# Kernel optimization log

Measured on AMD Instinct MI355X. Metric: run time of the kernel, lower is better.

Reference implementation:

```python
import jax, jax.numpy as jnp
from jax import lax
import numpy as np

# (cin, cout, kernel, pad) for the 18 convs (funs 1,3,5,6,7,9,10,11,13..17,19..23)
CONVS = [(3,32,3,0),(32,64,3,0),(64,128,3,1),(128,64,1,0),(64,128,3,1),
         (128,256,3,1),(256,128,1,0),(128,256,3,0),(256,512,3,1),(512,256,1,0),
         (256,512,3,1),(512,256,1,0),(256,512,3,0),(512,256,3,1),(256,128,1,0),
         (128,64,3,1),(64,32,1,0),(32,6,3,1)]
# maxpool(2,2) after conv index (1-based) -> pool padding (torch pads with -inf, floor mode)
POOL_AFTER = {1: 1, 2: 1, 5: 0, 8: 1, 13: 1}
GT = (0.567, 0.469, 0.206, 0.53)  # hardcoded ground-truth box (cx, cy, w, h), normalized


def _backbone(x, ws, bs):
    for i, (w, b) in enumerate(zip(ws, bs), 1):
        pad = CONVS[i - 1][3]
        x = lax.conv_general_dilated(
            x, w, (1, 1), [(pad, pad), (pad, pad)],
            dimension_numbers=("NCHW", "OIHW", "NCHW")) + b[None, :, None, None]
        if i in POOL_AFTER:
            p = POOL_AFTER[i]
            x = lax.reduce_window(
                x, -jnp.inf, lax.max, (1, 1, 2, 2), (1, 1, 2, 2),
                [(0, 0), (0, 0), (p, p), (p, p)])
    return x


def _head(x):
    # torch: x.transpose(1,3) on [B,6,H,W] -> [B,W,H,6]; j indexes W, k indexes H
    xt = jnp.transpose(x, (0, 3, 2, 1))
    B, W, H, _ = xt.shape
    j = jnp.arange(W, dtype=xt.dtype)[None, :, None]  # [1,W,1]
    k = jnp.arange(H, dtype=xt.dtype)[None, None, :]  # [1,1,H]
    px = (j + xt[..., 2]) / W
    py = (k + xt[..., 3]) / H
    pw = jnp.exp(xt[..., 4]) / W
    ph = jnp.exp(xt[..., 5]) / H
    # center-format IoU against the single gt box (detached mask, as in torch via float())
    iw = jnp.clip(jnp.minimum(px + pw * 0.5, GT[0] + GT[2] * 0.5)
                  - jnp.maximum(px - pw * 0.5, GT[0] - GT[2] * 0.5), 0.0)
    ih = jnp.clip(jnp.minimum(py + ph * 0.5, GT[1] + GT[3] * 0.5)
                  - jnp.maximum(py - ph * 0.5, GT[1] - GT[3] * 0.5), 0.0)
    inter = iw * ih
    iou = inter / (pw * ph + GT[2] * GT[3] - inter)
    iou = lax.stop_gradient(iou)
    tx = GT[0] * W - j          # [1,W,1]
    ty = GT[1] * H - k          # [1,1,H]
    tw = np.log(GT[2] * W).astype(np.float32)
    th = np.log(GT[3] * H).astype(np.float32)
    l1 = (jnp.abs(tx - xt[..., 2]) + jnp.abs(ty - xt[..., 3])
          + jnp.abs(tw - xt[..., 4]) + jnp.abs(th - xt[..., 5]))
    loss = jnp.sum(jnp.where(iou > 0.5, l1, 0.0)).reshape(1)
    return xt, loss


def setup_inputs() -> dict:
    key = jax.random.key(0)
    keys = jax.random.split(key, 1 + 2 * len(CONVS))
    d = {"x": jax.random.normal(keys[0], (16, 3, 416, 416), jnp.float32)}
    for i, (cin, cout, ks, _) in enumerate(CONVS, 1):
        fan_in = cin * ks * ks
        d[f"w{i}"] = jax.random.normal(keys[2 * i - 1], (cout, cin, ks, ks), jnp.float32) / np.sqrt(fan_in)
        d[f"b{i}"] = jax.random.normal(keys[2 * i], (cout,), jnp.float32) * 0.01
    return d


def reference(x, w1, b1, w2, b2, w3, b3, w4, b4, w5, b5, w6, b6, w7, b7, w8, b8,
              w9, b9, w10, b10, w11, b11, w12, b12, w13, b13, w14, b14, w15, b15,
              w16, b16, w17, b17, w18, b18):
    ws = [w1, w2, w3, w4, w5, w6, w7, w8, w9, w10, w11, w12, w13, w14, w15, w16, w17, w18]
    bs = [b1, b2, b3, b4, b5, b6, b7, b8, b9, b10, b11, b12, b13, b14, b15, b16, b17, b18]
    feat = _backbone(x, ws, bs)
    xt, loss = _head(feat)
    return (xt, loss)
```

## Files before the change

kernel.cpp:

```cpp
#include <hip/hip_runtime.h>
#include <math.h>

typedef short v8s __attribute__((ext_vector_type(8)));
typedef float v4f __attribute__((ext_vector_type(4)));

template<int K, int COT, bool POOL, bool MASK, bool SWAP>
__global__ __launch_bounds__(256) void conv_fused(
    const float* __restrict__ in, const float* __restrict__ wgt,
    const float* __restrict__ bias, float* __restrict__ out,
    int B, int Cin, int Hin, int Win,
    int Hc, int Wc, int Hout, int Wout,
    int Cout, int cpad, int ppad,
    int inPS, int inRS, int inOfs, int outPS, int outRS, int outOfs)
{
    constexpr int NPY = POOL ? 2 : 1;
    constexpr int PS  = K + NPY - 1;
    const int spatial = Hout * Wout;
    const int idx = (SWAP ? blockIdx.y : blockIdx.x) * blockDim.x + threadIdx.x;
    const int cog = SWAP ? blockIdx.x : blockIdx.y;
    const int total = B * spatial;
    if (idx >= total) return;
    const int b  = idx / spatial;
    const int sp = idx - b * spatial;
    const int oy = sp / Wout;
    const int ox = sp - oy * Wout;
    const int co0 = cog * COT;

    const int cy0 = POOL ? (2 * oy - ppad) : oy;
    const int cx0 = POOL ? (2 * ox - ppad) : ox;
    const int iy0 = cy0 - cpad;
    const int ix0 = cx0 - cpad;

    bool my[PS], mx[PS];
#pragma unroll
    for (int i = 0; i < PS; i++) {
        my[i] = !MASK || ((unsigned)(iy0 + i) < (unsigned)Hin);
        mx[i] = !MASK || ((unsigned)(ix0 + i) < (unsigned)Win);
    }

    float acc[COT][NPY * NPY];
#pragma unroll
    for (int c = 0; c < COT; c++)
#pragma unroll
        for (int p = 0; p < NPY * NPY; p++) acc[c][p] = 0.f;

    const float* inB = in + inOfs + (size_t)b * Cin * inPS;
    const long wBase  = (long)co0 * Cin * K * K;

    for (int ci = 0; ci < Cin; ci++) {
        const float* ip = inB + (size_t)ci * inPS;
        float patch[PS][PS];
#pragma unroll
        for (int py = 0; py < PS; py++) {
#pragma unroll
            for (int px = 0; px < PS; px++) {
                float v = 0.f;
                if (my[py] && mx[px]) v = ip[(iy0 + py) * inRS + (ix0 + px)];
                patch[py][px] = v;
            }
        }
        const float* wp = wgt + wBase + (long)ci * K * K;
#pragma unroll
        for (int c = 0; c < COT; c++) {
#pragma unroll
            for (int kh = 0; kh < K; kh++)
#pragma unroll
            for (int kw = 0; kw < K; kw++) {
                const float wv = wp[(long)c * Cin * K * K + kh * K + kw];
#pragma unroll
                for (int dy = 0; dy < NPY; dy++)
#pragma unroll
                for (int dx = 0; dx < NPY; dx++)
                    acc[c][dy * NPY + dx] = fmaf(wv, patch[dy + kh][dx + kw],
                                                 acc[c][dy * NPY + dx]);
            }
        }
    }

#pragma unroll
    for (int c = 0; c < COT; c++) {
        float v;
        if (POOL) {
            v = -INFINITY;
#pragma unroll
            for (int dy = 0; dy < NPY; dy++)
#pragma unroll
            for (int dx = 0; dx < NPY; dx++) {
                const int cy = cy0 + dy, cx = cx0 + dx;
                if ((unsigned)cy < (unsigned)Hc && (unsigned)cx < (unsigned)Wc)
                    v = fmaxf(v, acc[c][dy * NPY + dx]);
            }
        } else {
            v = acc[c][0];
        }
        v += bias[co0 + c];
        out[outOfs + (size_t)(b * Cout + co0 + c) * outPS + oy * outRS + ox] = v;
    }
}

__global__ __launch_bounds__(256) void ring_zero(
    float* __restrict__ buf, int planes, int H, int W)
{
    int Wp = W + 2, Hp = H + 2;
    int ringlen = 2 * Wp + 2 * H;
    int t = blockIdx.x * 256 + threadIdx.x;
    if (t >= planes * ringlen) return;
    int p = t / ringlen, r = t - p * ringlen;
    float* pl = buf + (size_t)p * Hp * Wp;
    int idx;
    if (r < Wp) idx = r;
    else if (r < 2 * Wp) idx = (Hp - 1) * Wp + (r - Wp);
    else { int rr = r - 2 * Wp; int row = 1 + (rr >> 1); idx = row * Wp + ((rr & 1) ? (Wp - 1) : 0); }
    pl[idx] = 0.f;
}

__device__ __forceinline__ unsigned short f2bf_rne(float x) {
    unsigned u = __float_as_uint(x);
    return (unsigned short)((u + 0x7fffu + ((u >> 16) & 1u)) >> 16);
}
__device__ __forceinline__ float bf2f(unsigned short h) {
    return __uint_as_float(((unsigned)h) << 16);
}

__global__ __launch_bounds__(256) void prepack(
    const float* __restrict__ w, unsigned short* __restrict__ hi,
    unsigned short* __restrict__ lo, int cout, int kdim, int nkb)
{
    int t = blockIdx.x * 256 + threadIdx.x;
    if (t >= cout * kdim) return;
    int co = t / kdim, k = t - co * kdim;
    int cb = co >> 4, m = co & 15, kb = k >> 5, kk = k & 31;
    int lane = ((kk >> 3) << 4) | m, j = kk & 7;
    long dst = ((long)(cb * nkb + kb) << 9) + lane * 8 + j;
    float x = w[t];
    unsigned short h = f2bf_rne(x);
    hi[dst] = h;
    lo[dst] = f2bf_rne(x - bf2f(h));
}

template<int MT, int KS, bool SPLIT>
__global__ __launch_bounds__(256) void conv_mfma(
    const float* __restrict__ in, const unsigned short* __restrict__ whi,
    const unsigned short* __restrict__ wlo, const float* __restrict__ bias,
    float* __restrict__ out, int Cin, int inHWp, int inWp, int Hc, int Wc,
    int Cout, int pad, int b0, int nb, int nkbTot, int nkbPer, int Mpad,
    int outHWp, int outWp)
{
    const int HW = Hc * Wc;
    const int M = nb * HW;
    const int tid = threadIdx.x;
    const int lane = tid & 63;
    const int wv = tid >> 6;
    const int spBase = blockIdx.x * 64;
    const int kb0 = SPLIT ? blockIdx.z * nkbPer : 0;
    const int kb1 = SPLIT ? kb0 + nkbPer : nkbTot;

    __shared__ unsigned short P[2][5120];

    const int spoL = lane >> 2;
    int kkc[2];
    kkc[0] = (tid & 3) + 4 * wv;
    kkc[1] = kkc[0] + 16;

    const float* sptr[4];
    int soff[4];
#pragma unroll
    for (int j = 0; j < 4; ++j) {
        int sp = spBase + spoL + 16 * j;
        int q = sp < M ? sp : M - 1;
        int b = q / HW; int r = q - b * HW;
        int soy = r / Wc, sox = r - soy * Wc;
        soff[j] = (soy + 1) * inWp + (sox + 1);
        sptr[j] = in + (size_t)(b0 + b) * Cin * inHWp;
    }

    int ci[2], r9[2], koff[2];
#pragma unroll
    for (int m = 0; m < 2; ++m) {
        int k = kb0 * 32 + kkc[m];
        if (KS == 3) {
            ci[m] = k / 9; r9[m] = k - 9 * ci[m];
            int d3 = (r9[m] >= 3) + (r9[m] >= 6);
            koff[m] = ci[m] * inHWp + (d3 - pad) * inWp + (r9[m] - 3 * d3 - pad);
        } else { ci[m] = k; koff[m] = k * inHWp; }
    }

    float rv[8];
#define STAGE()                                                                \
    {                                                                          \
        _Pragma("unroll")                                                      \
        for (int m = 0; m < 2; ++m)                                            \
        _Pragma("unroll")                                                      \
        for (int j = 0; j < 4; ++j)                                            \
            rv[m * 4 + j] = sptr[j][koff[m] + soff[j]];                        \
    }
#define ADVANCE()                                                              \
    {                                                                          \
        _Pragma("unroll")                                                      \
        for (int m = 0; m < 2; ++m) {                                          \
            if (KS == 3) {                                                     \
                r9[m] += 5; int c = r9[m] >= 9; r9[m] -= c ? 9 : 0;            \
                ci[m] += 3 + c;                                                \
                int d3 = (r9[m] >= 3) + (r9[m] >= 6);                          \
                koff[m] = ci[m] * inHWp + (d3 - pad) * inWp                    \
                        + (r9[m] - 3 * d3 - pad);                              \
            } else { koff[m] += 32 * inHWp; }                                  \
        }                                                                      \
    }

    STAGE();

    const int g0 = blockIdx.y * (MT * 4) + wv * MT;
    const unsigned short* whp[MT];
    const unsigned short* wlp[MT];
#pragma unroll
    for (int mt = 0; mt < MT; ++mt) {
        size_t base = (((size_t)(g0 + mt) * nkbTot + kb0) << 9) + lane * 8;
        whp[mt] = whi + base; wlp[mt] = wlo + base;
    }

    v4f acc[MT][4];
    {
        v4f z = {0.f, 0.f, 0.f, 0.f};
#pragma unroll
        for (int mt = 0; mt < MT; ++mt)
#pragma unroll
            for (int nt = 0; nt < 4; ++nt) acc[mt][nt] = z;
    }

    for (int kb = kb0; kb < kb1; ++kb) {
        unsigned short* Ph = P[kb & 1];
#pragma unroll
        for (int m = 0; m < 2; ++m)
#pragma unroll
        for (int j = 0; j < 4; ++j) {
            float v = rv[m * 4 + j];
            unsigned vb = __float_as_uint(v);
            float res = v - __uint_as_float(vb & 0xffff0000u);
            int a = (spoL + 16 * j) * 40 + kkc[m];
            Ph[a] = (unsigned short)(vb >> 16);
            Ph[2560 + a] = (unsigned short)(__float_as_uint(res) >> 16);
        }
        __syncthreads();

        v8s wh[MT], wl[MT];
#pragma unroll
        for (int mt = 0; mt < MT; ++mt) {
            wh[mt] = *(const v8s*)whp[mt];
            wl[mt] = *(const v8s*)wlp[mt];
            whp[mt] += 512; wlp[mt] += 512;
        }

        if (kb + 1 < kb1) { ADVANCE(); STAGE(); }

#pragma unroll
        for (int nt = 0; nt < 4; ++nt) {
            int ro = (nt * 16 + (lane & 15)) * 40 + (lane >> 4) * 8;
            v8s ph = *(const v8s*)(Ph + ro);
            v8s pl = *(const v8s*)(Ph + 2560 + ro);
#pragma unroll
            for (int mt = 0; mt < MT; ++mt) {
                acc[mt][nt] = __builtin_amdgcn_mfma_f32_16x16x32_bf16(wh[mt], ph, acc[mt][nt], 0, 0, 0);
                acc[mt][nt] = __builtin_amdgcn_mfma_f32_16x16x32_bf16(wh[mt], pl, acc[mt][nt], 0, 0, 0);
                acc[mt][nt] = __builtin_amdgcn_mfma_f32_16x16x32_bf16(wl[mt], ph, acc[mt][nt], 0, 0, 0);
            }
        }
    }
#undef STAGE
#undef ADVANCE

    const int qrow = (lane >> 4) * 4;
    if (SPLIT) {
        float* pz = out + (size_t)blockIdx.z * Cout * Mpad;
#pragma unroll
        for (int mt = 0; mt < MT; ++mt) {
            int co = (g0 + mt) * 16 + qrow;
#pragma unroll
            for (int nt = 0; nt < 4; ++nt) {
                int sp = spBase + nt * 16 + (lane & 15);
                if (sp < M) {
#pragma unroll
                    for (int r = 0; r < 4; ++r)
                        pz[(size_t)(co + r) * Mpad + sp] = acc[mt][nt][r];
                }
            }
        }
    } else {
#pragma unroll
        for (int mt = 0; mt < MT; ++mt) {
            int co = (g0 + mt) * 16 + qrow;
            float bsv[4];
#pragma unroll
            for (int r = 0; r < 4; ++r) bsv[r] = bias[co + r];
#pragma unroll
            for (int nt = 0; nt < 4; ++nt) {
                int sp = spBase + nt * 16 + (lane & 15);
                if (sp < M) {
                    int b = sp / HW, rsp = sp - b * HW;
                    int y = rsp / Wc, xx = rsp - y * Wc;
                    float* op = out + (size_t)(b * Cout + co) * outHWp
                              + (size_t)(y + 1) * outWp + (xx + 1);
#pragma unroll
                    for (int r = 0; r < 4; ++r)
                        op[(size_t)r * outHWp] = acc[mt][nt][r] + bsv[r];
                }
            }
        }
    }
}

__global__ __launch_bounds__(256) void sk_reduce(
    const float* __restrict__ part, const float* __restrict__ bias,
    float* __restrict__ out, int Cout, int HW, int Wc, int M, int Mpad, int SK,
    int outHWp, int outWp)
{
    int t = blockIdx.x * 256 + threadIdx.x;
    if (t >= Cout * M) return;
    int co = t / M, m = t - co * M;
    float s = bias[co];
    for (int k = 0; k < SK; ++k)
        s += part[((size_t)k * Cout + co) * Mpad + m];
    int b = m / HW, rsp = m - b * HW;
    int y = rsp / Wc, xx = rsp - y * Wc;
    out[(size_t)(b * Cout + co) * outHWp + (size_t)(y + 1) * outWp + (xx + 1)] = s;
}

__global__ __launch_bounds__(256) void maxpool_k(
    const float* __restrict__ in, float* __restrict__ out,
    int Hc, int Wc, int Hp, int Wp, int p, int total,
    int inHWp, int inWp, int outHWp, int outWp)
{
    int t = blockIdx.x * 256 + threadIdx.x;
    if (t >= total) return;
    int wp2 = Hp * Wp;
    int bc = t / wp2; int r = t - bc * wp2;
    int y = r / Wp, xx = r - y * Wp;
    int y0 = 2 * y - p, x0 = 2 * xx - p;
    const float* ip = in + (size_t)bc * inHWp;
    float v = -INFINITY;
#pragma unroll
    for (int dy = 0; dy < 2; ++dy)
#pragma unroll
    for (int dx = 0; dx < 2; ++dx) {
        int yy = y0 + dy, xc = x0 + dx;
        if ((unsigned)yy < (unsigned)Hc && (unsigned)xc < (unsigned)Wc)
            v = fmaxf(v, ip[(yy + 1) * inWp + (xc + 1)]);
    }
    out[(size_t)bc * outHWp + (size_t)(y + 1) * outWp + (xx + 1)] = v;
}

__global__ __launch_bounds__(1024) void head_kernel(
    const float* __restrict__ x, float* __restrict__ out, int B)
{
    const int W = 13, H = 13;
    const float gx = 0.567f, gy = 0.469f, gw = 0.206f, gh = 0.53f;
    const int tid = threadIdx.x;
    const int total = B * W * H;
    float lsum = 0.f;
    for (int i = tid; i < total; i += blockDim.x) {
        const int b = i / (W * H);
        const int r = i - b * W * H;
        const int j = r / H;
        const int k = r - j * H;
        float v[6];
#pragma unroll
        for (int c = 0; c < 6; c++) {
            v[c] = x[((b * 6 + c) * H + k) * W + j];
            out[((b * W + j) * H + k) * 6 + c] = v[c];
        }
        const float px = (j + v[2]) / (float)W;
        const float py = (k + v[3]) / (float)H;
        const float pw = expf(v[4]) / (float)W;
        const float ph = expf(v[5]) / (float)H;
        float iw = fminf(px + pw * 0.5f, gx + gw * 0.5f)
                 - fmaxf(px - pw * 0.5f, gx - gw * 0.5f);
        iw = fmaxf(iw, 0.f);
        float ih = fminf(py + ph * 0.5f, gy + gh * 0.5f)
                 - fmaxf(py - ph * 0.5f, gy - gh * 0.5f);
        ih = fmaxf(ih, 0.f);
        const float inter = iw * ih;
        const float iou = inter / (pw * ph + gw * gh - inter);
        const float tx = gx * W - (float)j;
        const float ty = gy * H - (float)k;
        const float tw = logf(gw * W);
        const float th = logf(gh * H);
        const float l1 = fabsf(tx - v[2]) + fabsf(ty - v[3])
                       + fabsf(tw - v[4]) + fabsf(th - v[5]);
        if (iou > 0.5f) lsum += l1;
    }
    __shared__ float red[1024];
    red[tid] = lsum;
    __syncthreads();
    for (int s = blockDim.x / 2; s > 0; s >>= 1) {
        if (tid < s) red[tid] += red[tid + s];
        __syncthreads();
    }
    if (tid == 0) out[total * 6] = red[0];
}

extern "C" void kernel_launch(void* const* d_in, const int* in_sizes, int n_in,
                              void* d_out, int out_size, void* d_ws, size_t ws_size,
                              hipStream_t stream)
{
    (void)in_sizes; (void)n_in; (void)out_size;
    const float* x = (const float*)d_in[0];
    const int B = 16;
    const size_t MB = 1024 * 1024;
    char* ws = (char*)d_ws;
    float* bufA = (float*)ws;
    float* bufB = (float*)(ws + 93 * MB);
    unsigned short* WHI = (unsigned short*)(ws + 141 * MB);
    unsigned short* WLO = (unsigned short*)(ws + 153 * MB);
    char* TEMP = ws + 165 * MB;
    const bool gemmOK = ws_size >= 166 * MB;
    const size_t tempAvail = ws_size > 165 * MB ? ws_size - 165 * MB : 0;

    static const struct { int cin, cout, ks, cpad, pool, ppad; } L[18] = {
        {3,  32, 3, 0, 1, 1}, {32, 64, 3, 0, 1, 1}, {64, 128, 3, 1, 0, 0},
        {128, 64, 1, 0, 0, 0}, {64, 128, 3, 1, 1, 0}, {128, 256, 3, 1, 0, 0},
        {256, 128, 1, 0, 0, 0}, {128, 256, 3, 0, 1, 1}, {256, 512, 3, 1, 0, 0},
        {512, 256, 1, 0, 0, 0}, {256, 512, 3, 1, 0, 0}, {512, 256, 1, 0, 0, 0},
        {256, 512, 3, 0, 1, 1}, {512, 256, 3, 1, 0, 0}, {256, 128, 1, 0, 0, 0},
        {128, 64, 3, 1, 0, 0}, {64, 32, 1, 0, 0, 0}, {32, 6, 3, 1, 0, 0}
    };
    static const bool RING[18] = {0,1,0,1,1,0,0,1,0,1,0,0,1,0,1,0,1,0};

    if (gemmOK) {
        size_t off = 0;
        for (int i = 1; i <= 15; ++i) {
            int kdim = L[i].cin * L[i].ks * L[i].ks;
            int n = L[i].cout * kdim;
            prepack<<<(n + 255) / 256, 256, 0, stream>>>(
                (const float*)d_in[2 * i + 1], WHI + off, WLO + off,
                L[i].cout, kdim, kdim / 32);
            off += (size_t)n;
        }
    }

    const float* cur = x;
    int Hin = 416, Win = 416;
    size_t woff = 0;

    for (int i = 0; i < 18; ++i) {
        const auto& l = L[i];
        const int Hc = Hin + 2 * l.cpad - l.ks + 1;
        const int Wc = Win + 2 * l.cpad - l.ks + 1;
        const int Hout = l.pool ? (Hc + 2 * l.ppad - 2) / 2 + 1 : Hc;
        const int Wout = l.pool ? (Wc + 2 * l.ppad - 2) / 2 + 1 : Wc;
        float* dst = (i % 2 == 0) ? bufA : bufB;
        const float* w  = (const float*)d_in[2 * i + 1];
        const float* bb = (const float*)d_in[2 * i + 2];
        const int kdim = l.cin * l.ks * l.ks;
        const int nkb = kdim / 32;

        const int inRS  = (i == 0) ? Win : (Win + 2);
        const int inPS  = (i == 0) ? Hin * Win : (Hin + 2) * (Win + 2);
        const int inOfs = (i == 0) ? 0 : (inRS + 1);
        const bool outPad = (i != 17);
        const int outRS  = outPad ? (Wout + 2) : Wout;
        const int outPS  = outPad ? (Hout + 2) * (Wout + 2) : Hout * Wout;
        const int outOfs = outPad ? (outRS + 1) : 0;
        const int tRS = Wc + 2, tPS = (Hc + 2) * (Wc + 2);

        if (RING[i]) {
            int planes = B * l.cout;
            int ringlen = 2 * (Wout + 2) + 2 * Hout;
            ring_zero<<<(planes * ringlen + 255) / 256, 256, 0, stream>>>(
                dst, planes, Hout, Wout);
        }

        int nb = 16;
        if (l.pool) {
            size_t perImg = (size_t)l.cout * tPS * 4;
            while (nb && perImg * (size_t)nb > tempAvail) nb >>= 1;
        }
        const bool useG = gemmOK && i >= 1 && i <= 15 && (!l.pool || nb >= 1);

        if (useG) {
            for (int b0 = 0; b0 < B; b0 += nb) {
                const int M = nb * Hc * Wc;
                const int gx = (M + 63) / 64;
                int MTv = (l.cout >= 256 && (long)gx * (l.cout / 256) >= 512) ? 4
                        : (l.cout >= 128 && (long)gx * (l.cout / 128) >= 512) ? 2 : 1;
                int gy = l.cout / (MTv * 64);
                int SK = 1;
                if (!l.pool && (long)gx * gy < 512) {
                    if (nkb % 4 == 0 && (size_t)4 * l.cout * gx * 64 * 4 <= tempAvail) SK = 4;
                    else if (nkb % 2 == 0 && (size_t)2 * l.cout * gx * 64 * 4 <= tempAvail) SK = 2;
                }
                const int nkbPer = nkb / SK;
                const int Mpad = gx * 64;
                float* gout = l.pool ? (float*)TEMP : (SK > 1 ? (float*)TEMP : dst);
                const int gHWp = l.pool ? tPS : (SK > 1 ? 0 : outPS);
                const int gWp  = l.pool ? tRS : (SK > 1 ? 0 : outRS);
                dim3 gr(gx, gy, SK);
#define GL(MTC, KSC, SPL)                                                      \
                conv_mfma<MTC, KSC, SPL><<<gr, 256, 0, stream>>>(              \
                    cur, WHI + woff, WLO + woff, bb, gout, l.cin, inPS, inRS,  \
                    Hc, Wc, l.cout, l.cpad, b0, nb, nkb, nkbPer, Mpad,         \
                    gHWp, gWp)
#define G2(MTC, KSC) do { if (SK > 1) GL(MTC, KSC, true); else GL(MTC, KSC, false); } while (0)
                if (MTv == 4)      { if (l.ks == 3) G2(4, 3); else G2(4, 1); }
                else if (MTv == 2) { if (l.ks == 3) G2(2, 3); else G2(2, 1); }
                else               { if (l.ks == 3) G2(1, 3); else G2(1, 1); }
#undef G2
#undef GL
                if (SK > 1) {
                    int tot = l.cout * M;
                    sk_reduce<<<(tot + 255) / 256, 256, 0, stream>>>(
                        (const float*)TEMP, bb, dst, l.cout, Hc * Wc, Wc, M,
                        Mpad, SK, outPS, outRS);
                }
                if (l.pool) {
                    int total = nb * l.cout * Hout * Wout;
                    maxpool_k<<<(total + 255) / 256, 256, 0, stream>>>(
                        (const float*)TEMP,
                        dst + (size_t)b0 * l.cout * outPS,
                        Hc, Wc, Hout, Wout, l.ppad, total, tPS, tRS, outPS, outRS);
                }
            }
        } else {
            const int spatial = Hout * Wout;
#define FL(KK, CC, PP, MM, SW)                                                 \
            conv_fused<KK, CC, PP, MM, SW><<<                                  \
                SW ? dim3(l.cout / CC, (B * spatial + 255) / 256)              \
                   : dim3((B * spatial + 255) / 256, l.cout / CC),             \
                256, 0, stream>>>(                                             \
                cur, w, bb, dst, B, l.cin, Hin, Win, Hc, Wc, Hout, Wout,       \
                l.cout, l.cpad, l.ppad, inPS, inRS, inOfs, outPS, outRS, outOfs)
            if (i == 0)                           FL(3, 8, true, true, true);
            else if (i == 16)                     FL(1, 8, false, false, false);
            else if (i == 17)                     FL(3, 6, false, false, false);
            else if (l.pool)                      FL(3, 4, true, true, false);
            else if (l.ks == 3)                   FL(3, 8, false, true, false);
            else                                  FL(1, 8, false, true, false);
#undef FL
        }

        if (i >= 1 && i <= 15) woff += (size_t)l.cout * kdim;
        cur = dst;
        Hin = Hout;
        Win = Wout;
    }

    head_kernel<<<1, 1024, 0, stream>>>(cur, (float*)d_out, B);
}
```

Measured before the change: 1.520 ms.

## Prefetch high weights a chunk ahead, pack LDS stores, rework tile and split-K selection

New measurement: 1.650 ms. +8.6%, slower.

```diff
diff --git a/kernel.cpp b/kernel.cpp
--- a/kernel.cpp
+++ b/kernel.cpp
@@ -157,27 +157,23 @@
 
     __shared__ unsigned short P[2][5120];
 
-    const int spoL = lane >> 2;
-    int kkc[2];
-    kkc[0] = (tid & 3) + 4 * wv;
-    kkc[1] = kkc[0] + 16;
-
-    const float* sptr[4];
-    int soff[4];
+    const int spo = lane >> 2;
+    const int kp  = (tid & 3) + 4 * wv;
+
+    int jbase[4];
 #pragma unroll
     for (int j = 0; j < 4; ++j) {
-        int sp = spBase + spoL + 16 * j;
+        int sp = spBase + spo + 16 * j;
         int q = sp < M ? sp : M - 1;
         int b = q / HW; int r = q - b * HW;
         int soy = r / Wc, sox = r - soy * Wc;
-        soff[j] = (soy + 1) * inWp + (sox + 1);
-        sptr[j] = in + (size_t)(b0 + b) * Cin * inHWp;
+        jbase[j] = (b0 + b) * Cin * inHWp + (soy + 1) * inWp + (sox + 1);
     }
 
     int ci[2], r9[2], koff[2];
 #pragma unroll
     for (int m = 0; m < 2; ++m) {
-        int k = kb0 * 32 + kkc[m];
+        int k = kb0 * 32 + 2 * kp + m;
         if (KS == 3) {
             ci[m] = k / 9; r9[m] = k - 9 * ci[m];
             int d3 = (r9[m] >= 3) + (r9[m] >= 6);
@@ -192,7 +188,7 @@
         for (int m = 0; m < 2; ++m)                                            \
         _Pragma("unroll")                                                      \
         for (int j = 0; j < 4; ++j)                                            \
-            rv[m * 4 + j] = sptr[j][koff[m] + soff[j]];                        \
+            rv[m * 4 + j] = in[jbase[j] + koff[m]];                            \
     }
 #define ADVANCE()                                                              \
     {                                                                          \
@@ -219,6 +215,10 @@
         whp[mt] = whi + base; wlp[mt] = wlo + base;
     }
 
+    v8s WHa[MT], WHb[MT];
+#pragma unroll
+    for (int mt = 0; mt < MT; ++mt) { WHa[mt] = *(const v8s*)whp[mt]; whp[mt] += 512; }
+
     v4f acc[MT][4];
     {
         v4f z = {0.f, 0.f, 0.f, 0.f};
@@ -228,44 +228,65 @@
             for (int nt = 0; nt < 4; ++nt) acc[mt][nt] = z;
     }
 
-    for (int kb = kb0; kb < kb1; ++kb) {
-        unsigned short* Ph = P[kb & 1];
-#pragma unroll
-        for (int m = 0; m < 2; ++m)
-#pragma unroll
-        for (int j = 0; j < 4; ++j) {
-            float v = rv[m * 4 + j];
-            unsigned vb = __float_as_uint(v);
-            float res = v - __uint_as_float(vb & 0xffff0000u);
-            int a = (spoL + 16 * j) * 40 + kkc[m];
-            Ph[a] = (unsigned short)(vb >> 16);
-            Ph[2560 + a] = (unsigned short)(__float_as_uint(res) >> 16);
-        }
-        __syncthreads();
-
-        v8s wh[MT], wl[MT];
-#pragma unroll
-        for (int mt = 0; mt < MT; ++mt) {
-            wh[mt] = *(const v8s*)whp[mt];
-            wl[mt] = *(const v8s*)wlp[mt];
-            whp[mt] += 512; wlp[mt] += 512;
-        }
-
-        if (kb + 1 < kb1) { ADVANCE(); STAGE(); }
-
-#pragma unroll
-        for (int nt = 0; nt < 4; ++nt) {
-            int ro = (nt * 16 + (lane & 15)) * 40 + (lane >> 4) * 8;
-            v8s ph = *(const v8s*)(Ph + ro);
-            v8s pl = *(const v8s*)(Ph + 2560 + ro);
-#pragma unroll
-            for (int mt = 0; mt < MT; ++mt) {
-                acc[mt][nt] = __builtin_amdgcn_mfma_f32_16x16x32_bf16(wh[mt], ph, acc[mt][nt], 0, 0, 0);
-                acc[mt][nt] = __builtin_amdgcn_mfma_f32_16x16x32_bf16(wh[mt], pl, acc[mt][nt], 0, 0, 0);
-                acc[mt][nt] = __builtin_amdgcn_mfma_f32_16x16x32_bf16(wl[mt], ph, acc[mt][nt], 0, 0, 0);
-            }
-        }
-    }
+#define CHUNK(WC, WN)                                                          \
+    {                                                                          \
+        unsigned short* Pl = P[kb & 1];                                        \
+        _Pragma("unroll")                                                      \
+        for (int j = 0; j < 4; ++j) {                                          \
+            unsigned vb0 = __float_as_uint(rv[j]);                             \
+            unsigned vb1 = __float_as_uint(rv[4 + j]);                         \
+            unsigned hiP = (vb0 >> 16) | (vb1 & 0xffff0000u);                  \
+            float r0 = rv[j]     - __uint_as_float(vb0 & 0xffff0000u);         \
+            float r1 = rv[4 + j] - __uint_as_float(vb1 & 0xffff0000u);         \
+            unsigned loP = (__float_as_uint(r0) >> 16)                         \
+                         | (__float_as_uint(r1) & 0xffff0000u);                \
+            int a = (spo + 16 * j) * 40 + 2 * kp;                              \
+            *(unsigned*)(Pl + a) = hiP;                                        \
+            *(unsigned*)(Pl + 2560 + a) = loP;                                 \
+        }                                                                      \
+        __syncthreads();                                                       \
+        v8s wl_[MT];                                                           \
+        _Pragma("unroll")                                                      \
+        for (int mt = 0; mt < MT; ++mt) {                                      \
+            wl_[mt] = *(const v8s*)wlp[mt]; wlp[mt] += 512;                    \
+        }                                                                      \
+        if (kb + 1 < kb1) {                                                    \
+            _Pragma("unroll")                                                  \
+            for (int mt = 0; mt < MT; ++mt) {                                  \
+                WN[mt] = *(const v8s*)whp[mt]; whp[mt] += 512;                 \
+            }                                                                  \
+            ADVANCE(); STAGE();                                                \
+        }                                                                      \
+        v8s phr[4];                                                            \
+        _Pragma("unroll")                                                      \
+        for (int nt = 0; nt < 4; ++nt) {                                       \
+            int ro = (nt * 16 + (lane & 15)) * 40 + (lane >> 4) * 8;           \
+            phr[nt] = *(const v8s*)(Pl + ro);                                  \
+            v8s plr = *(const v8s*)(Pl + 2560 + ro);                           \
+            _Pragma("unroll")                                                  \
+            for (int mt = 0; mt < MT; ++mt) {                                  \
+                acc[mt][nt] = __builtin_amdgcn_mfma_f32_16x16x32_bf16(         \
+                    WC[mt], phr[nt], acc[mt][nt], 0, 0, 0);                    \
+                acc[mt][nt] = __builtin_amdgcn_mfma_f32_16x16x32_bf16(         \
+                    WC[mt], plr, acc[mt][nt], 0, 0, 0);                        \
+            }                                                                  \
+        }                                                                      \
+        _Pragma("unroll")                                                      \
+        for (int nt = 0; nt < 4; ++nt)                                         \
+        _Pragma("unroll")                                                      \
+        for (int mt = 0; mt < MT; ++mt)                                        \
+            acc[mt][nt] = __builtin_amdgcn_mfma_f32_16x16x32_bf16(             \
+                wl_[mt], phr[nt], acc[mt][nt], 0, 0, 0);                       \
+    }
+
+    int kb = kb0;
+    for (;;) {
+        CHUNK(WHa, WHb);
+        if (++kb >= kb1) break;
+        CHUNK(WHb, WHa);
+        if (++kb >= kb1) break;
+    }
+#undef CHUNK
 #undef STAGE
 #undef ADVANCE
 
@@ -480,16 +501,21 @@
             for (int b0 = 0; b0 < B; b0 += nb) {
                 const int M = nb * Hc * Wc;
                 const int gx = (M + 63) / 64;
-                int MTv = (l.cout >= 256 && (long)gx * (l.cout / 256) >= 512) ? 4
-                        : (l.cout >= 128 && (long)gx * (l.cout / 128) >= 512) ? 2 : 1;
+                const int Mpad = gx * 64;
+                int MTv = (l.cout >= 256) ? 4 : (l.cout >= 128 ? 2 : 1);
                 int gy = l.cout / (MTv * 64);
                 int SK = 1;
-                if (!l.pool && (long)gx * gy < 512) {
-                    if (nkb % 4 == 0 && (size_t)4 * l.cout * gx * 64 * 4 <= tempAvail) SK = 4;
-                    else if (nkb % 2 == 0 && (size_t)2 * l.cout * gx * 64 * 4 <= tempAvail) SK = 2;
+                if (!l.pool) {
+                    while ((long)gx * gy * SK < 512 && SK < 16 &&
+                           nkb % (SK * 2) == 0 &&
+                           (size_t)(SK * 2) * l.cout * Mpad * 4 <= tempAvail)
+                        SK *= 2;
+                } else {
+                    while (MTv > 1 && (long)gx * gy < 512) {
+                        MTv >>= 1; gy = l.cout / (MTv * 64);
+                    }
                 }
                 const int nkbPer = nkb / SK;
-                const int Mpad = gx * 64;
                 float* gout = l.pool ? (float*)TEMP : (SK > 1 ? (float*)TEMP : dst);
                 const int gHWp = l.pool ? tPS : (SK > 1 ? 0 : outPS);
                 const int gWp  = l.pool ? tRS : (SK > 1 ? 0 : outRS);
```

## Add intra-block K-split across two wave groups with LDS reduction in MFMA conv

Applied to the files above, without the earlier changes.

New measurement: 1.583 ms. 4.1% more time.

```diff
diff --git a/kernel.cpp b/kernel.cpp
--- a/kernel.cpp
+++ b/kernel.cpp
@@ -138,8 +138,8 @@
     lo[dst] = f2bf_rne(x - bf2f(h));
 }
 
-template<int MT, int KS, bool SPLIT>
-__global__ __launch_bounds__(256) void conv_mfma(
+template<int MT, int KS, bool SPLIT, int KW>
+__global__ __launch_bounds__(256 * KW) void conv_mfma(
     const float* __restrict__ in, const unsigned short* __restrict__ whi,
     const unsigned short* __restrict__ wlo, const float* __restrict__ bias,
     float* __restrict__ out, int Cin, int inHWp, int inWp, int Hc, int Wc,
@@ -150,34 +150,34 @@
     const int M = nb * HW;
     const int tid = threadIdx.x;
     const int lane = tid & 63;
-    const int wv = tid >> 6;
+    const int tl  = tid & 255;
+    const int grp = tid >> 8;
+    const int wv  = (tid >> 6) & 3;
     const int spBase = blockIdx.x * 64;
     const int kb0 = SPLIT ? blockIdx.z * nkbPer : 0;
     const int kb1 = SPLIT ? kb0 + nkbPer : nkbTot;
-
-    __shared__ unsigned short P[2][5120];
-
-    const int spoL = lane >> 2;
-    int kkc[2];
-    kkc[0] = (tid & 3) + 4 * wv;
-    kkc[1] = kkc[0] + 16;
-
-    const float* sptr[4];
-    int soff[4];
+    const int half = (kb1 - kb0) / KW;
+    const int kb0g = kb0 + grp * half;
+
+    __shared__ unsigned short P[KW][2][5120];
+
+    const int spo = lane >> 2;
+    const int kp  = (tl & 3) + 4 * wv;
+
+    int jbase[4];
 #pragma unroll
     for (int j = 0; j < 4; ++j) {
-        int sp = spBase + spoL + 16 * j;
+        int sp = spBase + spo + 16 * j;
         int q = sp < M ? sp : M - 1;
         int b = q / HW; int r = q - b * HW;
         int soy = r / Wc, sox = r - soy * Wc;
-        soff[j] = (soy + 1) * inWp + (sox + 1);
-        sptr[j] = in + (size_t)(b0 + b) * Cin * inHWp;
+        jbase[j] = (b0 + b) * Cin * inHWp + (soy + 1) * inWp + (sox + 1);
     }
 
     int ci[2], r9[2], koff[2];
 #pragma unroll
     for (int m = 0; m < 2; ++m) {
-        int k = kb0 * 32 + kkc[m];
+        int k = kb0g * 32 + 2 * kp + m;
         if (KS == 3) {
             ci[m] = k / 9; r9[m] = k - 9 * ci[m];
             int d3 = (r9[m] >= 3) + (r9[m] >= 6);
@@ -192,7 +192,7 @@
         for (int m = 0; m < 2; ++m)                                            \
         _Pragma("unroll")                                                      \
         for (int j = 0; j < 4; ++j)                                            \
-            rv[m * 4 + j] = sptr[j][koff[m] + soff[j]];                        \
+            rv[m * 4 + j] = in[jbase[j] + koff[m]];                            \
     }
 #define ADVANCE()                                                              \
     {                                                                          \
@@ -215,7 +215,7 @@
     const unsigned short* wlp[MT];
 #pragma unroll
     for (int mt = 0; mt < MT; ++mt) {
-        size_t base = (((size_t)(g0 + mt) * nkbTot + kb0) << 9) + lane * 8;
+        size_t base = (((size_t)(g0 + mt) * nkbTot + kb0g) << 9) + lane * 8;
         whp[mt] = whi + base; wlp[mt] = wlo + base;
     }
 
@@ -228,36 +228,37 @@
             for (int nt = 0; nt < 4; ++nt) acc[mt][nt] = z;
     }
 
-    for (int kb = kb0; kb < kb1; ++kb) {
-        unsigned short* Ph = P[kb & 1];
-#pragma unroll
-        for (int m = 0; m < 2; ++m)
+    for (int cc = 0; cc < half; ++cc) {
+        unsigned short* Pl = (unsigned short*)P[grp][cc & 1];
 #pragma unroll
         for (int j = 0; j < 4; ++j) {
-            float v = rv[m * 4 + j];
-            unsigned vb = __float_as_uint(v);
-            float res = v - __uint_as_float(vb & 0xffff0000u);
-            int a = (spoL + 16 * j) * 40 + kkc[m];
-            Ph[a] = (unsigned short)(vb >> 16);
-            Ph[2560 + a] = (unsigned short)(__float_as_uint(res) >> 16);
+            unsigned vb0 = __float_as_uint(rv[j]);
+            unsigned vb1 = __float_as_uint(rv[4 + j]);
+            unsigned hiP = (vb0 >> 16) | (vb1 & 0xffff0000u);
+            float r0 = rv[j]     - __uint_as_float(vb0 & 0xffff0000u);
+            float r1 = rv[4 + j] - __uint_as_float(vb1 & 0xffff0000u);
+            unsigned loP = (__float_as_uint(r0) >> 16)
+                         | (__float_as_uint(r1) & 0xffff0000u);
+            int a = (spo + 16 * j) * 40 + 2 * kp;
+            *(unsigned*)(Pl + a) = hiP;
+            *(unsigned*)(Pl + 2560 + a) = loP;
         }
         __syncthreads();
 
         v8s wh[MT], wl[MT];
 #pragma unroll
         for (int mt = 0; mt < MT; ++mt) {
-            wh[mt] = *(const v8s*)whp[mt];
-            wl[mt] = *(const v8s*)wlp[mt];
-            whp[mt] += 512; wlp[mt] += 512;
-        }
-
-        if (kb + 1 < kb1) { ADVANCE(); STAGE(); }
+            wh[mt] = *(const v8s*)whp[mt]; whp[mt] += 512;
+            wl[mt] = *(const v8s*)wlp[mt]; wlp[mt] += 512;
+        }
+
+        if (cc + 1 < half) { ADVANCE(); STAGE(); }
 
 #pragma unroll
         for (int nt = 0; nt < 4; ++nt) {
             int ro = (nt * 16 + (lane & 15)) * 40 + (lane >> 4) * 8;
-            v8s ph = *(const v8s*)(Ph + ro);
-            v8s pl = *(const v8s*)(Ph + 2560 + ro);
+            v8s ph = *(const v8s*)(Pl + ro);
+            v8s pl = *(const v8s*)(Pl + 2560 + ro);
 #pragma unroll
             for (int mt = 0; mt < MT; ++mt) {
                 acc[mt][nt] = __builtin_amdgcn_mfma_f32_16x16x32_bf16(wh[mt], ph, acc[mt][nt], 0, 0, 0);
@@ -269,40 +270,66 @@
 #undef STAGE
 #undef ADVANCE
 
-    const int qrow = (lane >> 4) * 4;
-    if (SPLIT) {
-        float* pz = out + (size_t)blockIdx.z * Cout * Mpad;
-#pragma unroll
-        for (int mt = 0; mt < MT; ++mt) {
-            int co = (g0 + mt) * 16 + qrow;
-#pragma unroll
-            for (int nt = 0; nt < 4; ++nt) {
-                int sp = spBase + nt * 16 + (lane & 15);
-                if (sp < M) {
-#pragma unroll
-                    for (int r = 0; r < 4; ++r)
-                        pz[(size_t)(co + r) * Mpad + sp] = acc[mt][nt][r];
+    if (KW == 2) {
+        __syncthreads();
+        float* R = (float*)&P[0][0][0];
+        if (grp == 1) {
+#pragma unroll
+            for (int mt = 0; mt < MT; ++mt)
+#pragma unroll
+            for (int nt = 0; nt < 4; ++nt)
+#pragma unroll
+            for (int r = 0; r < 4; ++r)
+                R[((mt * 4 + nt) * 4 + r) * 256 + tl] = acc[mt][nt][r];
+        }
+        __syncthreads();
+        if (grp == 0) {
+#pragma unroll
+            for (int mt = 0; mt < MT; ++mt)
+#pragma unroll
+            for (int nt = 0; nt < 4; ++nt)
+#pragma unroll
+            for (int r = 0; r < 4; ++r)
+                acc[mt][nt][r] += R[((mt * 4 + nt) * 4 + r) * 256 + tl];
+        }
+    }
+
+    if (KW == 1 || grp == 0) {
+        const int qrow = (lane >> 4) * 4;
+        if (SPLIT) {
+            float* pz = out + (size_t)blockIdx.z * Cout * Mpad;
+#pragma unroll
+            for (int mt = 0; mt < MT; ++mt) {
+                int co = (g0 + mt) * 16 + qrow;
+#pragma unroll
+                for (int nt = 0; nt < 4; ++nt) {
+                    int sp = spBase + nt * 16 + (lane & 15);
+                    if (sp < M) {
+#pragma unroll
+                        for (int r = 0; r < 4; ++r)
+                            pz[(size_t)(co + r) * Mpad + sp] = acc[mt][nt][r];
+                    }
                 }
             }
-        }
-    } else {
-#pragma unroll
-        for (int mt = 0; mt < MT; ++mt) {
-            int co = (g0 + mt) * 16 + qrow;
-            float bsv[4];
-#pragma unroll
-            for (int r = 0; r < 4; ++r) bsv[r] = bias[co + r];
-#pragma unroll
-            for (int nt = 0; nt < 4; ++nt) {
-                int sp = spBase + nt * 16 + (lane & 15);
-                if (sp < M) {
-                    int b = sp / HW, rsp = sp - b * HW;
-                    int y = rsp / Wc, xx = rsp - y * Wc;
-                    float* op = out + (size_t)(b * Cout + co) * outHWp
-                              + (size_t)(y + 1) * outWp + (xx + 1);
-#pragma unroll
-                    for (int r = 0; r < 4; ++r)
-                        op[(size_t)r * outHWp] = acc[mt][nt][r] + bsv[r];
+        } else {
+#pragma unroll
+            for (int mt = 0; mt < MT; ++mt) {
+                int co = (g0 + mt) * 16 + qrow;
+                float bsv[4];
+#pragma unroll
+                for (int r = 0; r < 4; ++r) bsv[r] = bias[co + r];
+#pragma unroll
+                for (int nt = 0; nt < 4; ++nt) {
+                    int sp = spBase + nt * 16 + (lane & 15);
+                    if (sp < M) {
+                        int b = sp / HW, rsp = sp - b * HW;
+                        int y = rsp / Wc, xx = rsp - y * Wc;
+                        float* op = out + (size_t)(b * Cout + co) * outHWp
+                                  + (size_t)(y + 1) * outWp + (xx + 1);
+#pragma unroll
+                        for (int r = 0; r < 4; ++r)
+                            op[(size_t)r * outHWp] = acc[mt][nt][r] + bsv[r];
+                    }
                 }
             }
         }
@@ -480,30 +507,41 @@
             for (int b0 = 0; b0 < B; b0 += nb) {
                 const int M = nb * Hc * Wc;
                 const int gx = (M + 63) / 64;
-                int MTv = (l.cout >= 256 && (long)gx * (l.cout / 256) >= 512) ? 4
-                        : (l.cout >= 128 && (long)gx * (l.cout / 128) >= 512) ? 2 : 1;
+                const int Mpad = gx * 64;
+                int MTv = (l.cout >= 256) ? 4 : (l.cout >= 128 ? 2 : 1);
                 int gy = l.cout / (MTv * 64);
+                if (MTv == 4 && (long)gx * gy < 1024) { MTv = 2; gy = l.cout / 128; }
+                int KW = 1;
+                if ((long)gx * gy < 1024 && MTv <= 2 && nkb % 2 == 0) KW = 2;
                 int SK = 1;
-                if (!l.pool && (long)gx * gy < 512) {
-                    if (nkb % 4 == 0 && (size_t)4 * l.cout * gx * 64 * 4 <= tempAvail) SK = 4;
-                    else if (nkb % 2 == 0 && (size_t)2 * l.cout * gx * 64 * 4 <= tempAvail) SK = 2;
+                if (!l.pool && KW == 2 && MTv == 2) {
+                    while ((long)gx * gy * SK * KW < 512 && SK < 16 &&
+                           nkb % (SK * 2 * KW) == 0 &&
+                           (size_t)(SK * 2) * l.cout * (size_t)Mpad * 4 <= tempAvail)
+                        SK *= 2;
                 }
                 const int nkbPer = nkb / SK;
-                const int Mpad = gx * 64;
                 float* gout = l.pool ? (float*)TEMP : (SK > 1 ? (float*)TEMP : dst);
                 const int gHWp = l.pool ? tPS : (SK > 1 ? 0 : outPS);
                 const int gWp  = l.pool ? tRS : (SK > 1 ? 0 : outRS);
                 dim3 gr(gx, gy, SK);
-#define GL(MTC, KSC, SPL)                                                      \
-                conv_mfma<MTC, KSC, SPL><<<gr, 256, 0, stream>>>(              \
+#define GL(MTC, KSC, SPL, KWC)                                                 \
+                conv_mfma<MTC, KSC, SPL, KWC><<<gr, 256 * KWC, 0, stream>>>(   \
                     cur, WHI + woff, WLO + woff, bb, gout, l.cin, inPS, inRS,  \
                     Hc, Wc, l.cout, l.cpad, b0, nb, nkb, nkbPer, Mpad,         \
                     gHWp, gWp)
-#define G2(MTC, KSC) do { if (SK > 1) GL(MTC, KSC, true); else GL(MTC, KSC, false); } while (0)
-                if (MTv == 4)      { if (l.ks == 3) G2(4, 3); else G2(4, 1); }
-                else if (MTv == 2) { if (l.ks == 3) G2(2, 3); else G2(2, 1); }
-                else               { if (l.ks == 3) G2(1, 3); else G2(1, 1); }
-#undef G2
+                if (KW == 2) {
+                    if (MTv == 2) {
+                        if (SK > 1) { if (l.ks == 3) GL(2, 3, true, 2);  else GL(2, 1, true, 2); }
+                        else        { if (l.ks == 3) GL(2, 3, false, 2); else GL(2, 1, false, 2); }
+                    } else {
+                        if (l.ks == 3) GL(1, 3, false, 2); else GL(1, 1, false, 2);
+                    }
+                } else {
+                    if (MTv == 4)      { if (l.ks == 3) GL(4, 3, false, 1); else GL(4, 1, false, 1); }
+                    else if (MTv == 2) { if (l.ks == 3) GL(2, 3, false, 1); else GL(2, 1, false, 1); }
+                    else               { if (l.ks == 3) GL(1, 3, false, 1); else GL(1, 1, false, 1); }
+                }
 #undef GL
                 if (SK > 1) {
                     int tot = l.cout * M;
```
